# Optimization experiments

Hardware: AMD Instinct MI355X
Metric: run time of the kernel (lower is better)

The kernel has to match this reference:

```python
import jax, jax.numpy as jnp
import numpy as np

B, H, W, C = 32, 64, 64, 256
WS, SS, NH = 8, 4, 8  # window size, shift size, num heads
HD = C // NH
N = WS * WS  # tokens per window
NW = (H // WS) * (W // WS)  # windows per image


def _rel_pos_index():
    coords = np.stack(np.meshgrid(np.arange(WS), np.arange(WS), indexing='ij'))  # [2,ws,ws]
    cf = coords.reshape(2, -1)
    rel = (cf[:, :, None] - cf[:, None, :]).transpose(1, 2, 0)  # [N,N,2]
    rel[:, :, 0] += WS - 1
    rel[:, :, 1] += WS - 1
    rel[:, :, 0] *= 2 * WS - 1
    return rel.sum(-1)  # [N,N] ints in [0,(2ws-1)^2)


def _shift_mask():
    # Standard Swin SW-MSA mask: -100 where tokens come from different regions.
    img = np.zeros((H, W))
    cnt = 0
    for hs in (slice(0, -WS), slice(-WS, -SS), slice(-SS, None)):
        for ws_ in (slice(0, -WS), slice(-WS, -SS), slice(-SS, None)):
            img[hs, ws_] = cnt
            cnt += 1
    mw = img.reshape(H // WS, WS, W // WS, WS).transpose(0, 2, 1, 3).reshape(-1, N)  # [nW,N]
    diff = mw[:, None, :] - mw[:, :, None]
    return np.where(diff != 0, -100.0, 0.0).astype(np.float32)  # [nW,N,N]


_RPI = _rel_pos_index()
_MASK = jnp.asarray(_shift_mask())


def _ln(x, g, b, eps=1e-5):
    m = jnp.mean(x, axis=-1, keepdims=True)
    v = jnp.var(x, axis=-1, keepdims=True)
    return (x - m) * jax.lax.rsqrt(v + eps) * g + b


def setup_inputs() -> dict:
    key = jax.random.key(0)
    ks = jax.random.split(key, 8)
    f = lambda k, shape: jax.random.normal(k, shape, jnp.float32) * 0.02
    return {
        'x': jax.random.normal(ks[0], (B, H * W, C), jnp.float32),
        'norm1_g': jnp.ones((C,), jnp.float32),
        'norm1_b': jnp.zeros((C,), jnp.float32),
        'qkv_w': f(ks[1], (3 * C, C)),
        'qkv_b': jnp.zeros((3 * C,), jnp.float32),
        'rpb_table': f(ks[2], ((2 * WS - 1) ** 2, NH)),
        'proj_w': f(ks[3], (C, C)),
        'proj_b': jnp.zeros((C,), jnp.float32),
        'norm2_g': jnp.ones((C,), jnp.float32),
        'norm2_b': jnp.zeros((C,), jnp.float32),
        'fc1_w': f(ks[4], (4 * C, C)),
        'fc1_b': jnp.zeros((4 * C,), jnp.float32),
        'fc2_w': f(ks[5], (C, 4 * C)),
        'fc2_b': jnp.zeros((C,), jnp.float32),
    }


def reference(x, norm1_g, norm1_b, qkv_w, qkv_b, rpb_table, proj_w, proj_b,
              norm2_g, norm2_b, fc1_w, fc1_b, fc2_w, fc2_b):
    shortcut = x
    h = _ln(x, norm1_g, norm1_b).reshape(B, H, W, C)
    # cyclic shift
    h = jnp.roll(h, shift=(-SS, -SS), axis=(1, 2))
    # window partition -> [B*nW, N, C]
    h = h.reshape(B, H // WS, WS, W // WS, WS, C)
    h = h.transpose(0, 1, 3, 2, 4, 5).reshape(B * NW, N, C)
    # windowed multi-head attention with relative position bias + shift mask
    qkv = (h @ qkv_w.T + qkv_b).reshape(B * NW, N, 3, NH, HD)
    q, k, v = qkv[:, :, 0], qkv[:, :, 1], qkv[:, :, 2]  # [Bn, N, NH, HD]
    scale = HD ** -0.5
    attn = jnp.einsum('bqhd,bkhd->bhqk', q * scale, k)  # [Bn, NH, N, N]
    bias = rpb_table[_RPI.reshape(-1)].reshape(N, N, NH).transpose(2, 0, 1)  # [NH,N,N]
    attn = attn + bias[None]
    attn = attn.reshape(B, NW, NH, N, N) + _MASK[None, :, None]
    attn = jax.nn.softmax(attn.reshape(B * NW, NH, N, N), axis=-1)
    h = jnp.einsum('bhqk,bkhd->bqhd', attn, v).reshape(B * NW, N, C)
    h = h @ proj_w.T + proj_b
    # window reverse
    h = h.reshape(B, H // WS, W // WS, WS, WS, C)
    h = h.transpose(0, 1, 3, 2, 4, 5).reshape(B, H, W, C)
    # reverse cyclic shift
    h = jnp.roll(h, shift=(SS, SS), axis=(1, 2)).reshape(B, H * W, C)
    x = shortcut + h  # drop_path = identity in eval
    # MLP
    m = _ln(x, norm2_g, norm2_b)
    m = jax.nn.gelu(m @ fc1_w.T + fc1_b)
    m = m @ fc2_w.T + fc2_b
    return x + m
```

## Files before the change

kernel.cpp:

```cpp
#include <hip/hip_runtime.h>
#include <hip/hip_bf16.h>
#include <stdint.h>

using f16 = _Float16;
typedef _Float16 f16x8 __attribute__((ext_vector_type(8)));
typedef float f32x4 __attribute__((ext_vector_type(4)));

static constexpr int HW = 4096;
static constexpr int CC = 256;
static constexpr int ROWS = 131072;
static constexpr int ACH = 4;
static constexpr int AROWS = ROWS / ACH;
static constexpr int CWINS = AROWS / 64;
static constexpr int MCH = 4;
static constexpr int MROWS = ROWS / MCH;
static constexpr int SSH = 4;

static constexpr size_t OFF_WQ = 0;
static constexpr size_t OFF_WP = OFF_WQ + (size_t)768*256*2;
static constexpr size_t OFF_W1 = OFF_WP + (size_t)256*256*2;
static constexpr size_t OFF_W2 = OFF_W1 + (size_t)1024*256*2;
static constexpr size_t OFF_R1 = OFF_W2 + (size_t)256*1024*2;
static constexpr size_t OFF_R2 = OFF_R1 + (size_t)ROWS*CC*2;

__device__ __forceinline__ void gload16(void* lds, const void* g) {
    __builtin_amdgcn_global_load_lds(
        (const __attribute__((address_space(1))) unsigned int*)g,
        (__attribute__((address_space(3))) unsigned int*)lds, 16, 0, 0);
}

__global__ void k_cvt(const float* __restrict__ s, f16* __restrict__ d, int n) {
    int i = blockIdx.x * 256 + threadIdx.x;
    if (i < n) d[i] = (f16)s[i];
}

__global__ __launch_bounds__(256) void k_ln(const float* __restrict__ x,
                                            const float* __restrict__ g,
                                            const float* __restrict__ be,
                                            f16* __restrict__ dst, int rowbase) {
    int lrow = blockIdx.x * 4 + (threadIdx.x >> 6);
    int grow = rowbase + lrow;
    int lane = threadIdx.x & 63;
    int n = grow & 63, win = (grow >> 6) & 63, b = grow >> 12;
    int hh  = ((win >> 3) << 3) | (n >> 3);
    int wwc = ((win & 7) << 3) | (n & 7);
    int ho = (hh + SSH) & 63, wo = (wwc + SSH) & 63;
    size_t srow = (size_t)b * HW + ho * 64 + wo;
    float4 v = ((const float4*)(x + srow * CC))[lane];
    float s  = v.x + v.y + v.z + v.w;
    float s2 = v.x*v.x + v.y*v.y + v.z*v.z + v.w*v.w;
#pragma unroll
    for (int off = 32; off; off >>= 1) { s += __shfl_xor(s, off); s2 += __shfl_xor(s2, off); }
    float mean = s * (1.f/256.f);
    float rstd = rsqrtf(s2 * (1.f/256.f) - mean*mean + 1e-5f);
    float4 gv = ((const float4*)g)[lane];
    float4 bv = ((const float4*)be)[lane];
    f16 ob[4];
    ob[0] = (f16)((v.x-mean)*rstd*gv.x + bv.x);
    ob[1] = (f16)((v.y-mean)*rstd*gv.y + bv.y);
    ob[2] = (f16)((v.z-mean)*rstd*gv.z + bv.z);
    ob[3] = (f16)((v.w-mean)*rstd*gv.w + bv.w);
    *(uint2*)(dst + (size_t)lrow * CC + lane * 4) = *(const uint2*)ob;
}

template<int KDIM, int EPI>
__global__ __launch_bounds__(256) void k_gemm(const f16* __restrict__ A,
                                              const f16* __restrict__ Wt,
                                              const float* __restrict__ bias,
                                              int rowbase,
                                              float* outf, f16* __restrict__ outh,
                                              f16* __restrict__ q, f16* __restrict__ kk,
                                              f16* __restrict__ vv) {
    __shared__ f16 As[2][128 * 32];
    __shared__ f16 Bs[2][128 * 32];
    const int tid = threadIdx.x;
    const int m0 = blockIdx.x * 128, n0 = blockIdx.y * 128;
    const int wave = tid >> 6, lane = tid & 63;
    const int wm = (wave >> 1) * 64, wn = (wave & 1) * 64;
    const int lr = lane & 15, kq = lane >> 4;
    const int i0 = wave * 128 + lane;
    const int r0 = i0 >> 2, c0 = (i0 & 3) * 8;
    const int i1 = i0 + 64;
    const int r1 = i1 >> 2, c1 = (i1 & 3) * 8;
    const int base0 = wave * 1024, base1 = base0 + 512;

    auto stage = [&](int b, int k0) {
        gload16(&As[b][base0], &A [(size_t)(m0 + r0) * KDIM + k0 + c0]);
        gload16(&Bs[b][base0], &Wt[(size_t)(n0 + r0) * KDIM + k0 + c0]);
        gload16(&As[b][base1], &A [(size_t)(m0 + r1) * KDIM + k0 + c1]);
        gload16(&Bs[b][base1], &Wt[(size_t)(n0 + r1) * KDIM + k0 + c1]);
    };

    f32x4 acc[4][4];
#pragma unroll
    for (int i = 0; i < 4; i++)
#pragma unroll
        for (int j = 0; j < 4; j++) acc[i][j] = f32x4{0.f, 0.f, 0.f, 0.f};

    constexpr int KSTEPS = KDIM / 32;
    stage(0, 0);
    __syncthreads();
    for (int s = 0; s < KSTEPS; s++) {
        int cur = s & 1;
        if (s + 1 < KSTEPS) stage(cur ^ 1, (s + 1) * 32);
        f16x8 af[4], bfv[4];
#pragma unroll
        for (int i = 0; i < 4; i++) {
            af[i]  = *(const f16x8*)(&As[cur][(wm + i * 16 + lr) * 32 + kq * 8]);
            bfv[i] = *(const f16x8*)(&Bs[cur][(wn + i * 16 + lr) * 32 + kq * 8]);
        }
#pragma unroll
        for (int mi = 0; mi < 4; mi++)
#pragma unroll
            for (int ni = 0; ni < 4; ni++)
                acc[mi][ni] = __builtin_amdgcn_mfma_f32_16x16x32_f16(af[mi], bfv[ni], acc[mi][ni], 0, 0, 0);
        __syncthreads();
    }

#pragma unroll
    for (int mi = 0; mi < 4; mi++)
#pragma unroll
        for (int ni = 0; ni < 4; ni++)
#pragma unroll
            for (int j = 0; j < 4; j++) {
                int lrow = m0 + wm + mi * 16 + kq * 4 + j;
                int gcol = n0 + wn + ni * 16 + lr;
                float val = acc[mi][ni][j] + bias[gcol];
                if constexpr (EPI == 0) {
                    int s = gcol >> 8, h2 = (gcol >> 5) & 7, d = gcol & 31;
                    if (s == 0) val *= 0.1767766952966369f;
                    f16* dst = (s == 0) ? q : (s == 1 ? kk : vv);
                    int winl = lrow >> 6, n = lrow & 63;
                    dst[(((size_t)winl * 8 + h2) * 64 + n) * 32 + d] = (f16)val;
                } else if constexpr (EPI == 2) {
                    float z = 0.7978845608028654f * (val + 0.044715f * val * val * val);
                    float t = 1.f - 2.f / (__expf(2.f * z) + 1.f);
                    outh[(size_t)lrow * 1024 + gcol] = (f16)(0.5f * val * (1.f + t));
                } else {
                    size_t idx = (size_t)(rowbase + lrow) * CC + gcol;
                    outf[idx] = outf[idx] + val;
                }
            }
}

__global__ __launch_bounds__(256, 2) void k_proj(const f16* __restrict__ A,
                                                 const f16* __restrict__ Wt,
                                                 const float* __restrict__ bias,
                                                 const float* __restrict__ x_in,
                                                 float* __restrict__ outf,
                                                 f16* __restrict__ m_out,
                                                 const float* __restrict__ g2,
                                                 const float* __restrict__ b2) {
    __shared__ f16 As[2][64 * 32];
    __shared__ f16 Bs[2][256 * 32];
    __shared__ float rsum[4][64];
    __shared__ float rsq[4][64];
    const int tid = threadIdx.x;
    const int m0 = blockIdx.x * 64;
    const int wave = tid >> 6, lane = tid & 63;
    const int lr = lane & 15, kq = lane >> 4;
    const int ar = tid >> 2, ac = (tid & 3) * 8;

    auto stage = [&](int b, int k0) {
        gload16(&As[b][wave * 512], &A[(size_t)(m0 + ar) * CC + k0 + ac]);
#pragma unroll
        for (int r = 0; r < 4; r++)
            gload16(&Bs[b][(r * 256 + wave * 64) * 8],
                    &Wt[(size_t)(r * 64 + ar) * CC + k0 + ac]);
    };

    f32x4 acc[4][4];
#pragma unroll
    for (int i = 0; i < 4; i++)
#pragma unroll
        for (int j = 0; j < 4; j++) acc[i][j] = f32x4{0.f, 0.f, 0.f, 0.f};

    stage(0, 0);
    __syncthreads();
    for (int s = 0; s < 8; s++) {
        int cur = s & 1;
        if (s + 1 < 8) stage(cur ^ 1, (s + 1) * 32);
        f16x8 af[4], bfv[4];
#pragma unroll
        for (int i = 0; i < 4; i++) {
            af[i]  = *(const f16x8*)(&As[cur][(i * 16 + lr) * 32 + kq * 8]);
            bfv[i] = *(const f16x8*)(&Bs[cur][(wave * 64 + i * 16 + lr) * 32 + kq * 8]);
        }
#pragma unroll
        for (int mi = 0; mi < 4; mi++)
#pragma unroll
            for (int ni = 0; ni < 4; ni++)
                acc[mi][ni] = __builtin_amdgcn_mfma_f32_16x16x32_f16(af[mi], bfv[ni], acc[mi][ni], 0, 0, 0);
        __syncthreads();
    }

    int srows[4][4];
#pragma unroll
    for (int mi = 0; mi < 4; mi++)
#pragma unroll
        for (int j = 0; j < 4; j++) {
            int row = m0 + mi * 16 + kq * 4 + j;
            int n = row & 63, win = (row >> 6) & 63, b = row >> 12;
            int hh  = ((win >> 3) << 3) | (n >> 3);
            int wwc = ((win & 7) << 3) | (n & 7);
            int ho = (hh + SSH) & 63, wo = (wwc + SSH) & 63;
            srows[mi][j] = b * HW + ho * 64 + wo;
        }
    float bv[4], gv[4], b2v[4];
#pragma unroll
    for (int ni = 0; ni < 4; ni++) {
        int gcol = wave * 64 + ni * 16 + lr;
        bv[ni] = bias[gcol]; gv[ni] = g2[gcol]; b2v[ni] = b2[gcol];
    }
    float ps[4][4], qs[4][4];
#pragma unroll
    for (int mi = 0; mi < 4; mi++)
#pragma unroll
        for (int j = 0; j < 4; j++) { ps[mi][j] = 0.f; qs[mi][j] = 0.f; }
#pragma unroll
    for (int mi = 0; mi < 4; mi++)
#pragma unroll
        for (int ni = 0; ni < 4; ni++) {
            int gcol = wave * 64 + ni * 16 + lr;
#pragma unroll
            for (int j = 0; j < 4; j++) {
                size_t idx = (size_t)srows[mi][j] * CC + gcol;
                float v = acc[mi][ni][j] + bv[ni] + x_in[idx];
                acc[mi][ni][j] = v;
                outf[idx] = v;
                ps[mi][j] += v; qs[mi][j] += v * v;
            }
        }
#pragma unroll
    for (int off = 1; off < 16; off <<= 1)
#pragma unroll
        for (int mi = 0; mi < 4; mi++)
#pragma unroll
            for (int j = 0; j < 4; j++) {
                ps[mi][j] += __shfl_xor(ps[mi][j], off);
                qs[mi][j] += __shfl_xor(qs[mi][j], off);
            }
    if (lr == 0) {
#pragma unroll
        for (int mi = 0; mi < 4; mi++)
#pragma unroll
            for (int j = 0; j < 4; j++) {
                int rl = mi * 16 + kq * 4 + j;
                rsum[wave][rl] = ps[mi][j];
                rsq[wave][rl]  = qs[mi][j];
            }
    }
    __syncthreads();
    float mean_a[4][4], rstd_a[4][4];
#pragma unroll
    for (int mi = 0; mi < 4; mi++)
#pragma unroll
        for (int j = 0; j < 4; j++) {
            int rl = mi * 16 + kq * 4 + j;
            float s  = rsum[0][rl] + rsum[1][rl] + rsum[2][rl] + rsum[3][rl];
            float s2 = rsq[0][rl] + rsq[1][rl] + rsq[2][rl] + rsq[3][rl];
            float mean = s * (1.f/256.f);
            float var  = s2 * (1.f/256.f) - mean * mean;
            mean_a[mi][j] = mean;
            rstd_a[mi][j] = rsqrtf(var + 1e-5f);
        }
#pragma unroll
    for (int mi = 0; mi < 4; mi++)
#pragma unroll
        for (int ni = 0; ni < 4; ni++) {
            int gcol = wave * 64 + ni * 16 + lr;
#pragma unroll
            for (int j = 0; j < 4; j++) {
                float m = (acc[mi][ni][j] - mean_a[mi][j]) * rstd_a[mi][j] * gv[ni] + b2v[ni];
                m_out[(size_t)srows[mi][j] * CC + gcol] = (f16)m;
            }
        }
}

__global__ __launch_bounds__(64) void k_attn(const f16* __restrict__ q,
                                             const f16* __restrict__ kk,
                                             const f16* __restrict__ vv,
                                             const float* __restrict__ rpb,
                                             f16* __restrict__ aw, int winbase) {
    __shared__ char sm[17408];
    float* rl = (float*)(sm + 16384);
    const int wl = blockIdx.x >> 3, h = blockIdx.x & 7;
    const int lane = threadIdx.x;
    const int lr = lane & 15, kq = lane >> 4;
    const size_t base = ((size_t)wl * 8 + h) * 2048;

    for (int i = lane; i < 225; i += 64) rl[i] = rpb[i * 8 + h];

    {
        f16 vr[32];
        const uint4* vs = (const uint4*)(vv + base + lane * 32);
#pragma unroll
        for (int c = 0; c < 4; c++) *(uint4*)&vr[c * 8] = vs[c];
#pragma unroll
        for (int d = 0; d < 32; d++)
            *(f16*)(sm + 8192 + d * 128 + ((lane * 2) ^ ((d & 7) << 4))) = vr[d];
    }

    f16x8 kf[4], qf[4];
#pragma unroll
    for (int t = 0; t < 4; t++) {
        kf[t] = *(const f16x8*)(kk + base + (size_t)(t * 16 + lr) * 32 + kq * 8);
        qf[t] = *(const f16x8*)(q  + base + (size_t)(t * 16 + lr) * 32 + kq * 8);
    }

    f32x4 st[4][4];
#pragma unroll
    for (int mi = 0; mi < 4; mi++)
#pragma unroll
        for (int ni = 0; ni < 4; ni++) st[mi][ni] = f32x4{0.f, 0.f, 0.f, 0.f};
#pragma unroll
    for (int mi = 0; mi < 4; mi++)
#pragma unroll
        for (int ni = 0; ni < 4; ni++)
            st[mi][ni] = __builtin_amdgcn_mfma_f32_16x16x32_f16(kf[mi], qf[ni], st[mi][ni], 0, 0, 0);

    __syncthreads();

    const int gwin = (winbase + wl) & 63;
    const int wh = gwin >> 3, ww = gwin & 7;
    int yq[4], xq[4], rq[4];
#pragma unroll
    for (int ni = 0; ni < 4; ni++) {
        int qq = ni * 16 + lr;
        yq[ni] = qq >> 3; xq[ni] = qq & 7;
        rq[ni] = ((wh < 7) ? 0 : ((yq[ni] < 4) ? 1 : 2)) * 3 +
                 ((ww < 7) ? 0 : ((xq[ni] < 4) ? 1 : 2));
    }
#pragma unroll
    for (int mi = 0; mi < 4; mi++)
#pragma unroll
        for (int j = 0; j < 4; j++) {
            int kt = mi * 16 + kq * 4 + j;
            int yk = kt >> 3, xk = kt & 7;
            int rk = ((wh < 7) ? 0 : ((yk < 4) ? 1 : 2)) * 3 +
                     ((ww < 7) ? 0 : ((xk < 4) ? 1 : 2));
#pragma unroll
            for (int ni = 0; ni < 4; ni++) {
                float b = rl[(yq[ni] - yk + 7) * 15 + (xq[ni] - xk + 7)];
                if (rq[ni] != rk) b -= 100.f;
                st[mi][ni][j] += b;
            }
        }

    float mx[4] = {-1e30f, -1e30f, -1e30f, -1e30f};
#pragma unroll
    for (int mi = 0; mi < 4; mi++)
#pragma unroll
        for (int ni = 0; ni < 4; ni++)
#pragma unroll
            for (int j = 0; j < 4; j++) mx[ni] = fmaxf(mx[ni], st[mi][ni][j]);
#pragma unroll
    for (int ni = 0; ni < 4; ni++) {
        mx[ni] = fmaxf(mx[ni], __shfl_xor(mx[ni], 16));
        mx[ni] = fmaxf(mx[ni], __shfl_xor(mx[ni], 32));
    }
    float sme[4] = {0.f, 0.f, 0.f, 0.f};
#pragma unroll
    for (int mi = 0; mi < 4; mi++)
#pragma unroll
        for (int ni = 0; ni < 4; ni++)
#pragma unroll
            for (int j = 0; j < 4; j++) {
                float e = __expf(st[mi][ni][j] - mx[ni]);
                st[mi][ni][j] = e;
                sme[ni] += e;
            }
#pragma unroll
    for (int ni = 0; ni < 4; ni++) {
        sme[ni] += __shfl_xor(sme[ni], 16);
        sme[ni] += __shfl_xor(sme[ni], 32);
    }
    float inv[4];
#pragma unroll
    for (int ni = 0; ni < 4; ni++) inv[ni] = 1.f / sme[ni];

#pragma unroll
    for (int mi = 0; mi < 4; mi++)
#pragma unroll
        for (int ni = 0; ni < 4; ni++) {
            f16 t4[4];
#pragma unroll
            for (int j = 0; j < 4; j++) t4[j] = (f16)st[mi][ni][j];
            int qq = ni * 16 + lr;
            *(uint2*)(sm + qq * 128 + ((mi * 32 + kq * 8) ^ ((qq & 7) << 4))) =
                *(const uint2*)t4;
        }
    __syncthreads();

    f32x4 oa[2][4];
#pragma unroll
    for (int mi2 = 0; mi2 < 2; mi2++)
#pragma unroll
        for (int ni = 0; ni < 4; ni++) oa[mi2][ni] = f32x4{0.f, 0.f, 0.f, 0.f};
#pragma unroll
    for (int ks = 0; ks < 2; ks++) {
        f16x8 va[2], pb[4];
#pragma unroll
        for (int mi2 = 0; mi2 < 2; mi2++) {
            int row = mi2 * 16 + lr;
            va[mi2] = *(const f16x8*)(sm + 8192 + row * 128 +
                                      ((ks * 64 + kq * 16) ^ ((row & 7) << 4)));
        }
#pragma unroll
        for (int ni = 0; ni < 4; ni++) {
            int qq = ni * 16 + lr;
            pb[ni] = *(const f16x8*)(sm + qq * 128 +
                                     ((ks * 64 + kq * 16) ^ ((qq & 7) << 4)));
        }
#pragma unroll
        for (int mi2 = 0; mi2 < 2; mi2++)
#pragma unroll
            for (int ni = 0; ni < 4; ni++)
                oa[mi2][ni] = __builtin_amdgcn_mfma_f32_16x16x32_f16(va[mi2], pb[ni], oa[mi2][ni], 0, 0, 0);
    }

#pragma unroll
    for (int mi2 = 0; mi2 < 2; mi2++)
#pragma unroll
        for (int ni = 0; ni < 4; ni++) {
            f16 t4[4];
#pragma unroll
            for (int j = 0; j < 4; j++) t4[j] = (f16)(oa[mi2][ni][j] * inv[ni]);
            int qq = ni * 16 + lr;
            *(uint2*)(sm + 12288 + qq * 64 + ((mi2 * 32 + kq * 8) ^ ((qq & 3) << 4))) =
                *(const uint2*)t4;
        }
    __syncthreads();

    f16* dst = aw + ((size_t)(wl * 64 + lane)) * CC + h * 32;
#pragma unroll
    for (int c = 0; c < 4; c++) {
        uint4 wv = *(const uint4*)(sm + 12288 + lane * 64 +
                                   ((c * 16) ^ ((lane & 3) << 4)));
        *(uint4*)(dst + c * 8) = wv;
    }
}

extern "C" void kernel_launch(void* const* d_in, const int* in_sizes, int n_in,
                              void* d_out, int out_size, void* d_ws, size_t ws_size,
                              hipStream_t stream) {
    (void)in_sizes; (void)n_in; (void)out_size; (void)ws_size;
    const float* x      = (const float*)d_in[0];
    const float* g1     = (const float*)d_in[1];
    const float* b1     = (const float*)d_in[2];
    const float* qkv_w  = (const float*)d_in[3];
    const float* qkv_b  = (const float*)d_in[4];
    const float* rpb    = (const float*)d_in[5];
    const float* proj_w = (const float*)d_in[6];
    const float* proj_b = (const float*)d_in[7];
    const float* g2     = (const float*)d_in[8];
    const float* b2     = (const float*)d_in[9];
    const float* fc1_w  = (const float*)d_in[10];
    const float* fc1_b  = (const float*)d_in[11];
    const float* fc2_w  = (const float*)d_in[12];
    const float* fc2_b  = (const float*)d_in[13];
    float* out = (float*)d_out;
    char* ws = (char*)d_ws;
    f16* wq = (f16*)(ws + OFF_WQ);
    f16* wp = (f16*)(ws + OFF_WP);
    f16* w1 = (f16*)(ws + OFF_W1);
    f16* w2 = (f16*)(ws + OFF_W2);
    f16* awb = (f16*)(ws + OFF_R1);
    f16* mh  = (f16*)(ws + OFF_R1);
    static constexpr size_t QSZ = (size_t)CWINS * 8 * 64 * 32 * 2;
    f16* hwin = (f16*)(ws + OFF_R2);
    f16* qb   = (f16*)(ws + OFF_R2 + QSZ);
    f16* kb   = (f16*)(ws + OFF_R2 + 2 * QSZ);
    f16* vb   = (f16*)(ws + OFF_R2 + 3 * QSZ);
    f16* m_in = (f16*)(ws + OFF_R2);

    k_cvt<<<768, 256, 0, stream>>>(qkv_w, wq, 768 * 256);
    k_cvt<<<256, 256, 0, stream>>>(proj_w, wp, 256 * 256);
    k_cvt<<<1024, 256, 0, stream>>>(fc1_w, w1, 1024 * 256);
    k_cvt<<<1024, 256, 0, stream>>>(fc2_w, w2, 1024 * 256);

    for (int c = 0; c < ACH; c++) {
        k_ln<<<AROWS / 4, 256, 0, stream>>>(x, g1, b1, hwin, c * AROWS);
        k_gemm<256, 0><<<dim3(AROWS / 128, 6), 256, 0, stream>>>(
            hwin, wq, qkv_b, 0, nullptr, nullptr, qb, kb, vb);
        k_attn<<<CWINS * 8, 64, 0, stream>>>(
            qb, kb, vb, rpb, awb + (size_t)c * AROWS * CC, c * CWINS);
    }
    k_proj<<<ROWS / 64, 256, 0, stream>>>(awb, wp, proj_b, x, out, m_in, g2, b2);

    for (int c = 0; c < MCH; c++) {
        k_gemm<256, 2><<<dim3(MROWS / 128, 8), 256, 0, stream>>>(
            m_in + (size_t)c * MROWS * CC, w1, fc1_b, c * MROWS,
            nullptr, mh, nullptr, nullptr, nullptr);
        k_gemm<1024, 3><<<dim3(MROWS / 128, 2), 256, 0, stream>>>(
            mh, w2, fc2_b, c * MROWS, out, nullptr, nullptr, nullptr, nullptr);
    }
}
```

Measured before the change: 711.1 us.

## Fuse MLP fc1+GELU+fc2 into one kernel keeping hidden tile in LDS

Replaces the chunked fc1 GEMM (writing a 1024-wide f16 hidden activation to global memory) and the separate fc2 GEMM with a single kernel. Each block processes 64 rows, loops over 8 hidden slices of 128, computes fc1+GELU into a swizzled LDS buffer, then accumulates fc2 directly from LDS. This removes the global round-trip of the hidden activation and several launches, at the cost of smaller 64-row tiles, more barriers, and reduced per-block MFMA reuse for fc1.

```diff
diff --git a/kernel.cpp b/kernel.cpp
--- a/kernel.cpp
+++ b/kernel.cpp
@@ -12,8 +12,6 @@
 static constexpr int ACH = 4;
 static constexpr int AROWS = ROWS / ACH;
 static constexpr int CWINS = AROWS / 64;
-static constexpr int MCH = 4;
-static constexpr int MROWS = ROWS / MCH;
 static constexpr int SSH = 4;
 
 static constexpr size_t OFF_WQ = 0;
@@ -63,14 +61,11 @@
     *(uint2*)(dst + (size_t)lrow * CC + lane * 4) = *(const uint2*)ob;
 }
 
-template<int KDIM, int EPI>
-__global__ __launch_bounds__(256) void k_gemm(const f16* __restrict__ A,
-                                              const f16* __restrict__ Wt,
-                                              const float* __restrict__ bias,
-                                              int rowbase,
-                                              float* outf, f16* __restrict__ outh,
-                                              f16* __restrict__ q, f16* __restrict__ kk,
-                                              f16* __restrict__ vv) {
+__global__ __launch_bounds__(256) void k_qkv(const f16* __restrict__ A,
+                                             const f16* __restrict__ Wt,
+                                             const float* __restrict__ bias,
+                                             f16* __restrict__ q, f16* __restrict__ kk,
+                                             f16* __restrict__ vv) {
     __shared__ f16 As[2][128 * 32];
     __shared__ f16 Bs[2][128 * 32];
     const int tid = threadIdx.x;
@@ -85,10 +80,10 @@
     const int base0 = wave * 1024, base1 = base0 + 512;
 
     auto stage = [&](int b, int k0) {
-        gload16(&As[b][base0], &A [(size_t)(m0 + r0) * KDIM + k0 + c0]);
-        gload16(&Bs[b][base0], &Wt[(size_t)(n0 + r0) * KDIM + k0 + c0]);
-        gload16(&As[b][base1], &A [(size_t)(m0 + r1) * KDIM + k0 + c1]);
-        gload16(&Bs[b][base1], &Wt[(size_t)(n0 + r1) * KDIM + k0 + c1]);
+        gload16(&As[b][base0], &A [(size_t)(m0 + r0) * CC + k0 + c0]);
+        gload16(&Bs[b][base0], &Wt[(size_t)(n0 + r0) * CC + k0 + c0]);
+        gload16(&As[b][base1], &A [(size_t)(m0 + r1) * CC + k0 + c1]);
+        gload16(&Bs[b][base1], &Wt[(size_t)(n0 + r1) * CC + k0 + c1]);
     };
 
     f32x4 acc[4][4];
@@ -97,12 +92,11 @@
 #pragma unroll
         for (int j = 0; j < 4; j++) acc[i][j] = f32x4{0.f, 0.f, 0.f, 0.f};
 
-    constexpr int KSTEPS = KDIM / 32;
     stage(0, 0);
     __syncthreads();
-    for (int s = 0; s < KSTEPS; s++) {
+    for (int s = 0; s < 8; s++) {
         int cur = s & 1;
-        if (s + 1 < KSTEPS) stage(cur ^ 1, (s + 1) * 32);
+        if (s + 1 < 8) stage(cur ^ 1, (s + 1) * 32);
         f16x8 af[4], bfv[4];
 #pragma unroll
         for (int i = 0; i < 4; i++) {
@@ -126,20 +120,11 @@
                 int lrow = m0 + wm + mi * 16 + kq * 4 + j;
                 int gcol = n0 + wn + ni * 16 + lr;
                 float val = acc[mi][ni][j] + bias[gcol];
-                if constexpr (EPI == 0) {
-                    int s = gcol >> 8, h2 = (gcol >> 5) & 7, d = gcol & 31;
-                    if (s == 0) val *= 0.1767766952966369f;
-                    f16* dst = (s == 0) ? q : (s == 1 ? kk : vv);
-                    int winl = lrow >> 6, n = lrow & 63;
-                    dst[(((size_t)winl * 8 + h2) * 64 + n) * 32 + d] = (f16)val;
-                } else if constexpr (EPI == 2) {
-                    float z = 0.7978845608028654f * (val + 0.044715f * val * val * val);
-                    float t = 1.f - 2.f / (__expf(2.f * z) + 1.f);
-                    outh[(size_t)lrow * 1024 + gcol] = (f16)(0.5f * val * (1.f + t));
-                } else {
-                    size_t idx = (size_t)(rowbase + lrow) * CC + gcol;
-                    outf[idx] = outf[idx] + val;
-                }
+                int s = gcol >> 8, h2 = (gcol >> 5) & 7, d = gcol & 31;
+                if (s == 0) val *= 0.1767766952966369f;
+                f16* dst = (s == 0) ? q : (s == 1 ? kk : vv);
+                int winl = lrow >> 6, n = lrow & 63;
+                dst[(((size_t)winl * 8 + h2) * 64 + n) * 32 + d] = (f16)val;
             }
 }
 
@@ -275,6 +260,126 @@
                 m_out[(size_t)srows[mi][j] * CC + gcol] = (f16)m;
             }
         }
+}
+
+__global__ __launch_bounds__(256) void k_mlp2(const f16* __restrict__ A,
+                                              const f16* __restrict__ w1,
+                                              const f16* __restrict__ w2,
+                                              const float* __restrict__ fb1,
+                                              const float* __restrict__ fb2,
+                                              float* __restrict__ out) {
+    __shared__ char sm[49152];
+    char* hbuf = sm;
+    char* S    = sm + 16384;
+    f16* As  = (f16*)S;
+    f16* Bs1 = (f16*)(S + 8192);
+    f16* Bs2 = (f16*)S;
+    const int tid = threadIdx.x, wave = tid >> 6, lane = tid & 63;
+    const int lr = lane & 15, kq = lane >> 4;
+    const int m0 = blockIdx.x * 64;
+    const int ar = tid >> 2, ac = (tid & 3) * 8;
+
+    f32x4 acc2[4][4];
+#pragma unroll
+    for (int i = 0; i < 4; i++)
+#pragma unroll
+        for (int j = 0; j < 4; j++) acc2[i][j] = f32x4{0.f, 0.f, 0.f, 0.f};
+
+    for (int nb = 0; nb < 8; nb++) {
+        auto stage1 = [&](int b, int k0) {
+            gload16(&As[b * 2048 + wave * 512], &A[(size_t)(m0 + ar) * CC + k0 + ac]);
+            gload16(&Bs1[b * 4096 + wave * 512],
+                    &w1[(size_t)(nb * 128 + ar) * CC + k0 + ac]);
+            gload16(&Bs1[b * 4096 + 2048 + wave * 512],
+                    &w1[(size_t)(nb * 128 + 64 + ar) * CC + k0 + ac]);
+        };
+        f32x4 acc1[4][2];
+#pragma unroll
+        for (int i = 0; i < 4; i++)
+#pragma unroll
+            for (int j = 0; j < 2; j++) acc1[i][j] = f32x4{0.f, 0.f, 0.f, 0.f};
+        stage1(0, 0);
+        __syncthreads();
+#pragma unroll
+        for (int ks = 0; ks < 8; ks++) {
+            int cur = ks & 1;
+            if (ks + 1 < 8) stage1(cur ^ 1, (ks + 1) * 32);
+            f16x8 af[4], bf[2];
+#pragma unroll
+            for (int mi = 0; mi < 4; mi++)
+                af[mi] = *(const f16x8*)(&As[cur * 2048 + (mi * 16 + lr) * 32 + kq * 8]);
+#pragma unroll
+            for (int ni = 0; ni < 2; ni++)
+                bf[ni] = *(const f16x8*)(&Bs1[cur * 4096 +
+                                              (wave * 32 + ni * 16 + lr) * 32 + kq * 8]);
+#pragma unroll
+            for (int mi = 0; mi < 4; mi++)
+#pragma unroll
+                for (int ni = 0; ni < 2; ni++)
+                    acc1[mi][ni] = __builtin_amdgcn_mfma_f32_16x16x32_f16(
+                        af[mi], bf[ni], acc1[mi][ni], 0, 0, 0);
+            __syncthreads();
+        }
+#pragma unroll
+        for (int ni = 0; ni < 2; ni++) {
+            int c = wave * 32 + ni * 16 + lr;
+            float bb = fb1[nb * 128 + c];
+#pragma unroll
+            for (int mi = 0; mi < 4; mi++)
+#pragma unroll
+                for (int j = 0; j < 4; j++) {
+                    float v = acc1[mi][ni][j] + bb;
+                    float z = 0.7978845608028654f * (v + 0.044715f * v * v * v);
+                    float t = 1.f - 2.f / (__expf(2.f * z) + 1.f);
+                    float gl = 0.5f * v * (1.f + t);
+                    int r = mi * 16 + kq * 4 + j;
+                    *(f16*)(hbuf + r * 256 + ((2 * c) ^ ((r & 7) << 4))) = (f16)gl;
+                }
+        }
+        auto stage2 = [&](int b, int k0) {
+#pragma unroll
+            for (int t = 0; t < 4; t++)
+                gload16(&Bs2[b * 8192 + t * 2048 + wave * 512],
+                        &w2[(size_t)(t * 64 + ar) * 1024 + nb * 128 + k0 + ac]);
+        };
+        stage2(0, 0);
+        __syncthreads();
+#pragma unroll
+        for (int ks = 0; ks < 4; ks++) {
+            int cur = ks & 1;
+            if (ks + 1 < 4) stage2(cur ^ 1, (ks + 1) * 32);
+            f16x8 ah[4], bw[4];
+#pragma unroll
+            for (int mi = 0; mi < 4; mi++) {
+                int row = mi * 16 + lr;
+                ah[mi] = *(const f16x8*)(hbuf + row * 256 +
+                                         ((ks * 64 + kq * 16) ^ ((row & 7) << 4)));
+            }
+#pragma unroll
+            for (int ni = 0; ni < 4; ni++)
+                bw[ni] = *(const f16x8*)(&Bs2[cur * 8192 +
+                                              (wave * 64 + ni * 16 + lr) * 32 + kq * 8]);
+#pragma unroll
+            for (int mi = 0; mi < 4; mi++)
+#pragma unroll
+                for (int ni = 0; ni < 4; ni++)
+                    acc2[mi][ni] = __builtin_amdgcn_mfma_f32_16x16x32_f16(
+                        ah[mi], bw[ni], acc2[mi][ni], 0, 0, 0);
+            __syncthreads();
+        }
+    }
+
+#pragma unroll
+    for (int mi = 0; mi < 4; mi++)
+#pragma unroll
+        for (int ni = 0; ni < 4; ni++)
+#pragma unroll
+            for (int j = 0; j < 4; j++) {
+                int qrow = m0 + mi * 16 + kq * 4 + j;
+                int oc = wave * 64 + ni * 16 + lr;
+                size_t idx = (size_t)qrow * CC + oc;
+                out[idx] = out[idx] + acc2[mi][ni][j] + fb2[oc];
+            }
 }
 
 __global__ __launch_bounds__(64) void k_attn(const f16* __restrict__ q,
@@ -466,7 +571,6 @@
     f16* w1 = (f16*)(ws + OFF_W1);
     f16* w2 = (f16*)(ws + OFF_W2);
     f16* awb = (f16*)(ws + OFF_R1);
-    f16* mh  = (f16*)(ws + OFF_R1);
     static constexpr size_t QSZ = (size_t)CWINS * 8 * 64 * 32 * 2;
     f16* hwin = (f16*)(ws + OFF_R2);
     f16* qb   = (f16*)(ws + OFF_R2 + QSZ);
@@ -481,18 +585,12 @@
 
     for (int c = 0; c < ACH; c++) {
         k_ln<<<AROWS / 4, 256, 0, stream>>>(x, g1, b1, hwin, c * AROWS);
-        k_gemm<256, 0><<<dim3(AROWS / 128, 6), 256, 0, stream>>>(
-            hwin, wq, qkv_b, 0, nullptr, nullptr, qb, kb, vb);
+        k_qkv<<<dim3(AROWS / 128, 6), 256, 0, stream>>>(
+            hwin, wq, qkv_b, qb, kb, vb);
         k_attn<<<CWINS * 8, 64, 0, stream>>>(
             qb, kb, vb, rpb, awb + (size_t)c * AROWS * CC, c * CWINS);
     }
     k_proj<<<ROWS / 64, 256, 0, stream>>>(awb, wp, proj_b, x, out, m_in, g2, b2);
 
-    for (int c = 0; c < MCH; c++) {
-        k_gemm<256, 2><<<dim3(MROWS / 128, 8), 256, 0, stream>>>(
-            m_in + (size_t)c * MROWS * CC, w1, fc1_b, c * MROWS,
-            nullptr, mh, nullptr, nullptr, nullptr);
-        k_gemm<1024, 3><<<dim3(MROWS / 128, 2), 256, 0, stream>>>(
-            mh, w2, fc2_b, c * MROWS, out, nullptr, nullptr, nullptr, nullptr);
-    }
-}
+    k_mlp2<<<ROWS / 64, 256, 0, stream>>>(m_in, w1, w2, fc1_b, fc2_b, out);
+}
```

Result: faster. 627.9 us (-11.7%).
